# Performance work log

Measured on AMD Instinct MI355X. Metric: run time of the kernel, lower is better.

## Reference

```python
import jax, jax.numpy as jnp
import numpy as np

N_NODES, N_EDGES, F_IN, F_OUT = 10000, 320000, 256, 256


def setup_inputs() -> dict:
    key = jax.random.key(0)
    k1, k2, k3, k4, k5, k6 = jax.random.split(key, 6)
    feature = jax.random.normal(k1, (N_NODES, F_IN), jnp.float32)
    ew = jax.random.uniform(k2, (N_EDGES,), jnp.float32)          # edge weights
    src = jax.random.randint(k3, (N_EDGES,), 0, N_NODES)
    dst = jax.random.randint(k4, (N_EDGES,), 0, N_NODES)
    # nn.Linear(2*in_feats, out_feats): weight [out, 2*in], bias [out]
    W = jax.random.normal(k5, (F_OUT, 2 * F_IN), jnp.float32) / np.sqrt(2 * F_IN)
    b = jax.random.normal(k6, (F_OUT,), jnp.float32) * 0.01
    return {"feature": feature, "ew": ew, "src": src, "dst": dst, "W": W, "b": b}


def reference(feature, ew, src, dst, W, b):
    n = feature.shape[0]
    # edge_msg2: m[e] = h[src[0]] * h[src[e]] * w[e]   -> [E, F]
    msg = feature[src[0]] * feature[src] * ew[:, None]
    # reduce: segment mean over incoming edges (mailbox mean). The original
    # reduce also computes a segment max concatenated into 'hm', but the apply
    # module only consumes the mean half ('hm_mean', Linear in = 2*in_feats),
    # so the max is dead compute and omitted.
    sums = jax.ops.segment_sum(msg, dst, num_segments=n)
    cnt = jax.ops.segment_sum(jnp.ones((msg.shape[0],), msg.dtype), dst, num_segments=n)
    hm_mean = sums / jnp.maximum(cnt, 1.0)[:, None]
    # NodeApplyModule: relu(Linear(cat(h, hm_mean)))
    x = jnp.concatenate([feature, hm_mean], axis=1)  # [N, 2F]
    return jax.nn.relu(x @ W.T + b)
```

## Files before the change

kernel.cpp:

```cpp
#include <hip/hip_runtime.h>

#define N_NODES 10000
#define N_EDGES 320000
#define F 256
#define K2 512
#define HSLOT 48
#define SLOTS 96
#define CSTR 16
#define W_BLOCKS 128
#define CNT_BLOCKS 313
#define CONV_BLOCKS 2500
#define PREP_BLOCKS (W_BLOCKS + CNT_BLOCKS + CONV_BLOCKS)
#define K2_BLOCKS 1875
#define N_TILE16 625

typedef __attribute__((ext_vector_type(8))) __bf16 bf16x8;
typedef __attribute__((ext_vector_type(4))) __bf16 bf16x4;
typedef __attribute__((ext_vector_type(4))) float f32x4;
typedef __attribute__((ext_vector_type(2))) float f32x2;
typedef unsigned long long u64;
typedef unsigned int u32;
typedef unsigned short u16;


__global__ __launch_bounds__(256) void prep_conv_kernel(
    const float* __restrict__ feat,
    const float* __restrict__ Wm,
    const int* __restrict__ src,
    __bf16* __restrict__ Wt,
    int* __restrict__ cnt,
    u32* __restrict__ feat8) {
  int b = blockIdx.x;
  int tid = threadIdx.x;
  if (b < W_BLOCKS) {
    int idx = b * 256 + tid;
    int o_ = idx >> 7;
    int k = (idx & 127) * 4;
    float4 w = ((const float4*)Wm)[idx];
    if (k >= F) {
      int s0 = src[0];
      float4 h = ((const float4*)(feat + (size_t)s0 * F))[(k - F) >> 2];
      w.x *= h.x; w.y *= h.y; w.z *= h.z; w.w *= h.w;
    }
    bf16x4 o;
    o[0] = (__bf16)w.x; o[1] = (__bf16)w.y; o[2] = (__bf16)w.z; o[3] = (__bf16)w.w;
    int t = k >> 5, kq = (k & 31) >> 3, e = k & 7;
    size_t offT = (((size_t)t * 4 + kq) * 256 + o_) * 8 + e;
    *(bf16x4*)(Wt + offT) = o;
  } else if (b < W_BLOCKS + CNT_BLOCKS) {
    int idx = (b - W_BLOCKS) * 256 + tid;
    if (idx < 2 * N_NODES * CSTR / 4) ((int4*)cnt)[idx] = make_int4(0, 0, 0, 0);
  } else {
    int idx = (b - W_BLOCKS - CNT_BLOCKS) * 256 + tid;
    float4 v = ((const float4*)feat)[idx];
    u32 r8 = 0;
    r8 = __builtin_amdgcn_cvt_pk_fp8_f32(v.x, v.y, r8, false);
    r8 = __builtin_amdgcn_cvt_pk_fp8_f32(v.z, v.w, r8, true);
    feat8[idx] = r8;
  }
}

__global__ __launch_bounds__(256) void scatter_gemmA_kernel(
    const float* __restrict__ feat,
    const int* __restrict__ src,
    const int* __restrict__ dst,
    const float* __restrict__ ew,
    int* __restrict__ cnt,
    u32* __restrict__ bucket,
    const __bf16* __restrict__ Wt,
    const float* __restrict__ bias,
    float* __restrict__ out) {
  int b = blockIdx.x;
  int tid = threadIdx.x;
  int r3 = b % 3;
  if (r3 != 2) {
    int sid = (b / 3) * 2 + r3;
    int e = sid * 256 + tid;
    if (e >= N_EDGES) return;
    int d = dst[e];
    int par = e & 1;
    u32 wb = (__float_as_uint(ew[e]) + 0x8000u) & 0xFFFF0000u;
    int p = atomicAdd(&cnt[(d * 2 + par) * CSTR], 1);
    if (p < HSLOT) bucket[(size_t)d * SLOTS + par * HSLOT + p] = wb | (u32)src[e];
  } else {
    int mt = b / 3;
    const int wave = tid >> 6;
    const int lane = tid & 63;
    const int r15 = lane & 15;
    const int kq = lane >> 4;
    const int col0 = wave * 64;
    const int m0 = mt * 16;
    const float* arow = feat + (size_t)(m0 + r15) * F;

    f32x4 acc[4];
#pragma unroll
    for (int cs = 0; cs < 4; ++cs) acc[cs] = (f32x4){0.f, 0.f, 0.f, 0.f};

#pragma unroll
    for (int t = 0; t < 8; ++t) {
      float4 lo = *(const float4*)(arow + t * 32 + kq * 8);
      float4 hi = *(const float4*)(arow + t * 32 + kq * 8 + 4);
      bf16x8 a;
      a[0] = (__bf16)lo.x; a[1] = (__bf16)lo.y; a[2] = (__bf16)lo.z; a[3] = (__bf16)lo.w;
      a[4] = (__bf16)hi.x; a[5] = (__bf16)hi.y; a[6] = (__bf16)hi.z; a[7] = (__bf16)hi.w;
#pragma unroll
      for (int cs = 0; cs < 4; ++cs) {
        bf16x8 bb = *(const bf16x8*)(Wt + (((size_t)t * 4 + kq) * 256 + col0 + cs * 16 + r15) * 8);
        acc[cs] = __builtin_amdgcn_mfma_f32_16x16x32_bf16(a, bb, acc[cs], 0, 0, 0);
      }
    }

    const int rbase = kq * 4;
#pragma unroll
    for (int cs = 0; cs < 4; ++cs) {
      int col = col0 + cs * 16 + r15;
      float bv = bias[col];
#pragma unroll
      for (int r = 0; r < 4; ++r) {
        int orow = m0 + rbase + r;
        out[(size_t)orow * F + col] = acc[cs][r] + bv;
      }
    }
  }
}

__global__ __launch_bounds__(256) void node_agg_kernel(
    const u32* __restrict__ feat8,
    const u32* __restrict__ bucket,
    const int* __restrict__ cnt,
    __bf16* __restrict__ aggb) {
  int node = (blockIdx.x * 256 + threadIdx.x) >> 6;
  int lane = threadIdx.x & 63;
  if (node >= N_NODES) return;
  int c0 = cnt[(node * 2) * CSTR];
  int c1 = cnt[(node * 2 + 1) * CSTR];
  int cc0 = min(c0, HSLOT);
  int cc1 = min(c1, HSLOT);
  int cc = cc0 + cc1;
  int c = c0 + c1;
  const u32* bk = bucket + (size_t)node * SLOTS;
  const uint2* frow = (const uint2*)feat8;
  const int half = lane >> 5;
  const int slot = lane & 31;

  float acc[8];
#pragma unroll
  for (int e = 0; e < 8; ++e) acc[e] = 0.f;

  for (int i = 0; i < cc; i += 16) {
    u32 p[8];
    uint2 v[8];
#pragma unroll
    for (int j = 0; j < 8; ++j) {
      int e = i + half + 2 * j;
      int ec = min(e, cc - 1);
      int si = (ec < cc0) ? ec : (ec - cc0 + HSLOT);
      p[j] = bk[si];
    }
#pragma unroll
    for (int j = 0; j < 8; ++j)
      v[j] = frow[(size_t)(p[j] & 0xFFFFu) * 32 + slot];
#pragma unroll
    for (int j = 0; j < 8; ++j) {
      int e = i + half + 2 * j;
      float w = (e < cc) ? __uint_as_float(p[j] & 0xFFFF0000u) : 0.f;
      f32x2 f01 = __builtin_amdgcn_cvt_pk_f32_fp8(v[j].x, false);
      f32x2 f23 = __builtin_amdgcn_cvt_pk_f32_fp8(v[j].x, true);
      f32x2 f45 = __builtin_amdgcn_cvt_pk_f32_fp8(v[j].y, false);
      f32x2 f67 = __builtin_amdgcn_cvt_pk_f32_fp8(v[j].y, true);
      acc[0] += f01[0] * w; acc[1] += f01[1] * w;
      acc[2] += f23[0] * w; acc[3] += f23[1] * w;
      acc[4] += f45[0] * w; acc[5] += f45[1] * w;
      acc[6] += f67[0] * w; acc[7] += f67[1] * w;
    }
  }

#pragma unroll
  for (int e = 0; e < 8; ++e) acc[e] += __shfl_xor(acc[e], 32, 64);

  if (half == 0) {
    float ic = 1.0f / (float)max(c, 1);
    bf16x8 o;
#pragma unroll
    for (int e = 0; e < 8; ++e) o[e] = (__bf16)(acc[e] * ic);
    *(bf16x8*)(aggb + (size_t)node * F + slot * 8) = o;
  }
}

__global__ __launch_bounds__(256) void gemmB_kernel(
    const __bf16* __restrict__ aggb,
    const __bf16* __restrict__ Wt,
    float* __restrict__ out) {
  const int tid = threadIdx.x;
  const int wave = tid >> 6;
  const int lane = tid & 63;
  const int r15 = lane & 15;
  const int kq = lane >> 4;
  const int col0 = wave * 64;
  const int m0 = blockIdx.x * 16;

  const __bf16* arow = aggb + (size_t)(m0 + r15) * F;

  f32x4 acc[4];
#pragma unroll
  for (int cs = 0; cs < 4; ++cs) acc[cs] = (f32x4){0.f, 0.f, 0.f, 0.f};

#pragma unroll
  for (int t2 = 0; t2 < 8; ++t2) {
    bf16x8 a = *(const bf16x8*)(arow + t2 * 32 + kq * 8);
#pragma unroll
    for (int cs = 0; cs < 4; ++cs) {
      bf16x8 bb = *(const bf16x8*)(Wt + (((size_t)(t2 + 8) * 4 + kq) * 256 + col0 + cs * 16 + r15) * 8);
      acc[cs] = __builtin_amdgcn_mfma_f32_16x16x32_bf16(a, bb, acc[cs], 0, 0, 0);
    }
  }

  const int rbase = kq * 4;
#pragma unroll
  for (int cs = 0; cs < 4; ++cs) {
    int col = col0 + cs * 16 + r15;
#pragma unroll
    for (int r = 0; r < 4; ++r) {
      int orow = m0 + rbase + r;
      size_t oi = (size_t)orow * F + col;
      out[oi] = fmaxf(out[oi] + acc[cs][r], 0.0f);
    }
  }
}

extern "C" void kernel_launch(void* const* d_in, const int* in_sizes, int n_in,
                              void* d_out, int out_size, void* d_ws, size_t ws_size,
                              hipStream_t stream) {
  const float* feat = (const float*)d_in[0];
  const float* ew   = (const float*)d_in[1];
  const int*   src  = (const int*)d_in[2];
  const int*   dst  = (const int*)d_in[3];
  const float* Wm   = (const float*)d_in[4];
  const float* bias = (const float*)d_in[5];
  float* out = (float*)d_out;

  u32*    bucket = (u32*)d_ws;
  __bf16* aggb   = (__bf16*)(bucket + (size_t)N_NODES * SLOTS);
  __bf16* Wt     = aggb + (size_t)N_NODES * F;
  u32*    feat8  = (u32*)(Wt + (size_t)F * K2);
  int*    cnt    = (int*)(feat8 + (size_t)N_NODES * F / 4);

  prep_conv_kernel<<<PREP_BLOCKS, 256, 0, stream>>>(feat, Wm, src, Wt, cnt, feat8);
  scatter_gemmA_kernel<<<K2_BLOCKS, 256, 0, stream>>>(feat, src, dst, ew,
                                                      cnt, bucket, Wt, bias, out);
  node_agg_kernel<<<(N_NODES * 64 + 255) / 256, 256, 0, stream>>>(feat8, bucket, cnt, aggb);
  gemmB_kernel<<<N_TILE16, 256, 0, stream>>>(aggb, Wt, out);
}
```

Before: 55.30 us.

## Partition edge bucket counters per XCD with workgroup-scope atomics

The scatter phase now reads the hardware XCC id and gives each of the 8 XCDs its own per-node counter and 32-slot bucket region, in place of two parity halves. Because a counter is only touched by one XCD, the atomic increment can use workgroup scope, which lets it be handled in the XCD-local L2 rather than as a device-coherent atomic. The aggregation kernel reads 8 counters per node and maps each edge index to its XCD segment through a prefix-sum select chain. In exchange, the bucket array grows to 256 slots per node and the node kernel does more index arithmetic. Correctness relies on the scheduler placement never letting two XCDs share a counter, and on the XCD-local L2 results reaching memory before the next kernel runs.

After: 63.15 us. 14.2% more time.

```diff
diff --git a/kernel.cpp b/kernel.cpp
--- a/kernel.cpp
+++ b/kernel.cpp
@@ -4,9 +4,10 @@
 #define N_EDGES 320000
 #define F 256
 #define K2 512
-#define HSLOT 48
-#define SLOTS 96
-#define CSTR 16
+#define XCDS 8
+#define SLOTS_X 32
+#define NSLOT (XCDS * SLOTS_X)
+#define CSTR 4
 #define W_BLOCKS 128
 #define CNT_BLOCKS 313
 #define CONV_BLOCKS 2500
@@ -49,7 +50,7 @@
     *(bf16x4*)(Wt + offT) = o;
   } else if (b < W_BLOCKS + CNT_BLOCKS) {
     int idx = (b - W_BLOCKS) * 256 + tid;
-    if (idx < 2 * N_NODES * CSTR / 4) ((int4*)cnt)[idx] = make_int4(0, 0, 0, 0);
+    if (idx < XCDS * N_NODES * CSTR / 4) ((int4*)cnt)[idx] = make_int4(0, 0, 0, 0);
   } else {
     int idx = (b - W_BLOCKS - CNT_BLOCKS) * 256 + tid;
     float4 v = ((const float4*)feat)[idx];
@@ -74,14 +75,18 @@
   int tid = threadIdx.x;
   int r3 = b % 3;
   if (r3 != 2) {
+    u32 xcd;
+    asm volatile("s_getreg_b32 %0, hwreg(HW_REG_XCC_ID)" : "=s"(xcd));
+    xcd &= (XCDS - 1);
     int sid = (b / 3) * 2 + r3;
     int e = sid * 256 + tid;
     if (e >= N_EDGES) return;
     int d = dst[e];
-    int par = e & 1;
     u32 wb = (__float_as_uint(ew[e]) + 0x8000u) & 0xFFFF0000u;
-    int p = atomicAdd(&cnt[(d * 2 + par) * CSTR], 1);
-    if (p < HSLOT) bucket[(size_t)d * SLOTS + par * HSLOT + p] = wb | (u32)src[e];
+    int p = __hip_atomic_fetch_add(&cnt[((size_t)xcd * N_NODES + d) * CSTR], 1,
+                                   __ATOMIC_RELAXED, __HIP_MEMORY_SCOPE_WORKGROUP);
+    if (p < SLOTS_X)
+      bucket[(size_t)d * NSLOT + xcd * SLOTS_X + p] = wb | (u32)src[e];
   } else {
     int mt = b / 3;
     const int wave = tid >> 6;
@@ -132,13 +137,22 @@
   int node = (blockIdx.x * 256 + threadIdx.x) >> 6;
   int lane = threadIdx.x & 63;
   if (node >= N_NODES) return;
-  int c0 = cnt[(node * 2) * CSTR];
-  int c1 = cnt[(node * 2 + 1) * CSTR];
-  int cc0 = min(c0, HSLOT);
-  int cc1 = min(c1, HSLOT);
-  int cc = cc0 + cc1;
-  int c = c0 + c1;
-  const u32* bk = bucket + (size_t)node * SLOTS;
+  int c0 = cnt[((size_t)0 * N_NODES + node) * CSTR];
+  int c1 = cnt[((size_t)1 * N_NODES + node) * CSTR];
+  int c2 = cnt[((size_t)2 * N_NODES + node) * CSTR];
+  int c3 = cnt[((size_t)3 * N_NODES + node) * CSTR];
+  int c4 = cnt[((size_t)4 * N_NODES + node) * CSTR];
+  int c5 = cnt[((size_t)5 * N_NODES + node) * CSTR];
+  int c6 = cnt[((size_t)6 * N_NODES + node) * CSTR];
+  int c7 = cnt[((size_t)7 * N_NODES + node) * CSTR];
+  int q0 = min(c0, SLOTS_X), q1 = min(c1, SLOTS_X), q2 = min(c2, SLOTS_X),
+      q3 = min(c3, SLOTS_X), q4 = min(c4, SLOTS_X), q5 = min(c5, SLOTS_X),
+      q6 = min(c6, SLOTS_X), q7 = min(c7, SLOTS_X);
+  int P1 = q0, P2 = P1 + q1, P3 = P2 + q2, P4 = P3 + q3,
+      P5 = P4 + q4, P6 = P5 + q5, P7 = P6 + q6;
+  int cc = P7 + q7;
+  int c = c0 + c1 + c2 + c3 + c4 + c5 + c6 + c7;
+  const u32* bk = bucket + (size_t)node * NSLOT;
   const uint2* frow = (const uint2*)feat8;
   const int half = lane >> 5;
   const int slot = lane & 31;
@@ -154,8 +168,15 @@
     for (int j = 0; j < 8; ++j) {
       int e = i + half + 2 * j;
       int ec = min(e, cc - 1);
-      int si = (ec < cc0) ? ec : (ec - cc0 + HSLOT);
-      p[j] = bk[si];
+      int base = 0, sub = 0;
+      if (ec >= P1) { base = 1 * SLOTS_X; sub = P1; }
+      if (ec >= P2) { base = 2 * SLOTS_X; sub = P2; }
+      if (ec >= P3) { base = 3 * SLOTS_X; sub = P3; }
+      if (ec >= P4) { base = 4 * SLOTS_X; sub = P4; }
+      if (ec >= P5) { base = 5 * SLOTS_X; sub = P5; }
+      if (ec >= P6) { base = 6 * SLOTS_X; sub = P6; }
+      if (ec >= P7) { base = 7 * SLOTS_X; sub = P7; }
+      p[j] = bk[base + ec - sub];
     }
 #pragma unroll
     for (int j = 0; j < 8; ++j)
@@ -240,7 +261,7 @@
   float* out = (float*)d_out;
 
   u32*    bucket = (u32*)d_ws;
-  __bf16* aggb   = (__bf16*)(bucket + (size_t)N_NODES * SLOTS);
+  __bf16* aggb   = (__bf16*)(bucket + (size_t)N_NODES * NSLOT);
   __bf16* Wt     = aggb + (size_t)N_NODES * F;
   u32*    feat8  = (u32*)(Wt + (size_t)F * K2);
   int*    cnt    = (int*)(feat8 + (size_t)N_NODES * F / 4);
```
